# Kernel tuning notes

Measured on AMD Instinct MI355X. Metric: run time of the kernel, lower is better.

The kernel has to match this reference:

```python
import jax, jax.numpy as jnp
import numpy as np
from jax import lax

B, C_IN, C_OUT, K, H, W, NUM = 32, 256, 256, 3, 28, 28, 8


def setup_inputs() -> dict:
    key = jax.random.key(0)
    k1, k2, k3 = jax.random.split(key, 3)
    inputs = jax.random.normal(k1, (B, C_IN, H, W), dtype=jnp.float32)
    inputs_se = jax.random.uniform(k2, (B, NUM), dtype=jnp.float32)
    # weight bank [out*in*k*k, num], init scale sqrt(1/(c*k*k)) as in the module
    scale = np.sqrt(1.0 / (C_IN * K * K)).astype(np.float32)
    weight = jax.random.normal(k3, (C_OUT * C_IN * K * K, NUM), dtype=jnp.float32) * scale
    bias = jnp.zeros((C_OUT,), dtype=jnp.float32)
    return {"inputs": inputs, "inputs_se": inputs_se, "weight": weight, "bias": bias}


def reference(inputs, inputs_se, weight, bias):
    b, c, h, w = inputs.shape
    out_ch = bias.shape[0]
    # per-sample filter generation: [B, num] @ [num, out*in*k*k] -> [B, out, in, k, k]
    wgen = jnp.einsum('bn,on->bo', inputs_se, weight).reshape(b, out_ch, c, K, K)

    def conv_one(x, wk):
        # x: [C,H,W], wk: [O,C,K,K] -> [O,H,W]  (stride 1, padding 1)
        return lax.conv_general_dilated(
            x[None], wk,
            window_strides=(1, 1), padding=[(1, 1), (1, 1)],
            dimension_numbers=('NCHW', 'OIHW', 'NCHW'))[0]

    out = jax.vmap(conv_one)(inputs, wgen)  # [B, O, H, W]
    return out + bias[None, :, None, None]
```

## Files before the change

kernel.cpp:

```cpp
#include <hip/hip_runtime.h>
#include <hip/hip_fp16.h>

#define BB    32
#define CIN   256
#define COUT  256
#define HH    28
#define WW    28
#define NPIX  784
#define HP    30
#define WP    30

#define BM    64
#define BN    128
#define NT    7

#define SLICE_ELEMS 294912
#define WGEN_ELEMS  ((size_t)BB * 2 * SLICE_ELEMS)
#define XPAD_OFF    (WGEN_ELEMS)

#define PREP_GENW  256
#define PREP_GENX  960
#define PREP_GRID  (PREP_GENW + PREP_GENX)

typedef _Float16 f16x8 __attribute__((ext_vector_type(8)));
typedef float    f32x4 __attribute__((ext_vector_type(4)));

static __device__ __forceinline__ ushort f2h_bits(float v) {
    __half h = __float2half(v);
    return *reinterpret_cast<ushort*>(&h);
}

static __device__ __forceinline__ void gll16(const ushort* g, ushort* l) {
    __builtin_amdgcn_global_load_lds(
        (const __attribute__((address_space(1))) unsigned int*)g,
        (__attribute__((address_space(3))) unsigned int*)l, 16, 0, 0);
}

__global__ __launch_bounds__(256) void prep(const float* __restrict__ weight,
                                            const float* __restrict__ se,
                                            const float* __restrict__ x,
                                            ushort* __restrict__ wgen2,
                                            ushort* __restrict__ xpad) {
    __shared__ __align__(16) char smem[29696];
    const int bid = blockIdx.x;
    const int tid = threadIdx.x;

    if (bid < PREP_GENW) {
        const int og  = bid >> 3;
        const int c32 = bid & 7;
        const int ol  = tid >> 5;
        const int cl  = tid & 31;
        const int o   = og * 8 + ol;
        const int c   = c32 * 32 + cl;

        float*  se_sh = (float*)smem;
        ushort* w_lds = (ushort*)(smem + 1024);

        se_sh[tid] = se[tid];

        float4 wr[18];
        const float4* wp = (const float4*)(weight + ((size_t)o * CIN + c) * 72);
#pragma unroll
        for (int i = 0; i < 18; ++i) wr[i] = wp[i];

        const int khw0 = tid >> 5;
        const int q0   = (tid >> 3) & 3;
        const int ol0  = tid & 7;
        const int khw1 = 8;
        const int q1   = (tid >> 3) & 3;
        const int ol1  = tid & 7;
        const int o0   = og * 8 + ol0;
        const int sub0 = (o0 >> 4) & 7, col0 = o0 & 15;
        const int o1   = og * 8 + ol1;
        const int sub1 = (o1 >> 4) & 7, col1 = o1 & 15;
        const int mt0  = o0 >> 7;
        const int dst0 = ((c32 * 9 + khw0) * 512 + sub0 * 64 + q0 * 16 + col0) * 8;
        const int dst1 = ((c32 * 9 + khw1) * 512 + sub1 * 64 + q1 * 16 + col1) * 8;
        const int src0 = (khw0 * 8 + ol0) * 40 + q0 * 8;
        const int src1 = (khw1 * 8 + ol1) * 40 + q1 * 8;

        __syncthreads();

        for (int b = 0; b < BB; ++b) {
            const float s0 = se_sh[b * 8 + 0], s1 = se_sh[b * 8 + 1];
            const float s2 = se_sh[b * 8 + 2], s3 = se_sh[b * 8 + 3];
            const float s4 = se_sh[b * 8 + 4], s5 = se_sh[b * 8 + 5];
            const float s6 = se_sh[b * 8 + 6], s7 = se_sh[b * 8 + 7];
#pragma unroll
            for (int k = 0; k < 9; ++k) {
                const float4 w0 = wr[2 * k + 0];
                const float4 w1 = wr[2 * k + 1];
                const float v = w0.x * s0 + w0.y * s1 + w0.z * s2 + w0.w * s3
                              + w1.x * s4 + w1.y * s5 + w1.z * s6 + w1.w * s7;
                w_lds[(k * 8 + ol) * 40 + cl] = f2h_bits(v);
            }
            __syncthreads();
            ushort* slice_base = wgen2 + (size_t)(b * 2 + mt0) * SLICE_ELEMS;
            *(uint4*)(slice_base + dst0) = *(const uint4*)(w_lds + src0);
            if (tid < 32)
                *(uint4*)(slice_base + dst1) = *(const uint4*)(w_lds + src1);
            __syncthreads();
        }
    } else {
        const int idx = bid - PREP_GENW;
        const int hp  = idx % HP;
        const int b   = idx / HP;
        ushort* row = xpad + ((size_t)b * HP + hp) * WP * CIN;

        if (hp == 0 || hp == HP - 1) {
            uint* r32 = (uint*)row;
            for (int i = tid; i < (WP * CIN) / 2; i += 256) r32[i] = 0u;
            return;
        }
        {
            uint* c0 = (uint*)row;
            uint* c1 = (uint*)(row + (WP - 1) * CIN);
            if (tid < 128)       c0[tid] = 0u;
            else                 c1[tid - 128] = 0u;
        }
        float* lds = (float*)smem;
        const int h = hp - 1;
        const float* xr = x + (size_t)b * CIN * NPIX + h * WW;

        for (int f = tid; f < CIN * WW; f += 256) {
            const int c = f / WW;
            const int w = f % WW;
            lds[c * (WW + 1) + w] = xr[(size_t)c * NPIX + w];
        }
        __syncthreads();
        for (int g2 = tid; g2 < WW * CIN; g2 += 256) {
            const int w = g2 >> 8;
            const int c = g2 & 255;
            row[(w + 1) * CIN + c] = f2h_bits(lds[c * (WW + 1) + w]);
        }
    }
}

#define KOFF(k) (((k) / 3) * 30 + ((k) % 3))

__global__ __launch_bounds__(256, 4) void dconv_mfma(const ushort* __restrict__ wgen2,
                                                     const ushort* __restrict__ xpad,
                                                     const float* __restrict__ bias,
                                                     float* __restrict__ out) {
    const int bid    = blockIdx.x;
    const int g      = bid & 7;
    const int s      = bid >> 3;
    const int t      = s % 14;
    const int nt     = t % 7;
    const int mtl    = t / 7;
    const int slice2 = g + 8 * (s / 14);
    const int b      = slice2 >> 1;
    const int mtH    = slice2 & 1;

    const int tid  = threadIdx.x;
    const int lane = tid & 63;
    const int wave = tid >> 6;
    const int wm   = wave >> 1;
    const int wn   = wave & 1;
    const int col  = lane & 15;
    const int quad = lane >> 4;

    __shared__ ushort Psh[2][7680];

    const int mo   = mtH * 128 + mtl * 64 + wm * 32;
    const int no   = nt * BN + wn * 64;
    const int h_lo = (nt * BN) / WW;

    const f16x8* ag = (const f16x8*)(wgen2 + (size_t)slice2 * SLICE_ELEMS)
                      + (mtl * 4 + wm * 2) * 64 + lane;
    const ushort* xp = xpad + (size_t)b * HP * WP * CIN;

    int p_goff[4], p_loff[4];
    bool p_ok[4];
#pragma unroll
    for (int r = 0; r < 4; ++r) {
        const int j = r * 256 + tid;
        p_ok[r] = (j < 960);
        const int jj  = p_ok[r] ? j : 0;
        const int qc  = jj / 240;
        const int rem = jj % 240;
        const int rr  = rem / 30;
        const int ww  = rem % 30;
        int srow = h_lo + rr;
        if (srow > 29) srow = 29;
        p_goff[r] = (srow * WP + ww) * CIN + qc * 8;
        p_loff[r] = jj * 8;
    }

    int pixbase[4], pst[4];
#pragma unroll
    for (int j = 0; j < 4; ++j) {
        const int p  = no + j * 16 + col;
        pst[j] = p;
        const int pc = p > (NPIX - 1) ? (NPIX - 1) : p;
        pixbase[j] = (pc / WW - h_lo) * 30 + (pc % WW);
    }

    f32x4 acc[2][4];
#pragma unroll
    for (int mi = 0; mi < 2; ++mi)
#pragma unroll
        for (int nj = 0; nj < 4; ++nj)
            acc[mi][nj] = (f32x4){0.f, 0.f, 0.f, 0.f};

#pragma unroll
    for (int r = 0; r < 4; ++r)
        if (p_ok[r]) gll16(xp + p_goff[r], &Psh[0][p_loff[r]]);

    f16x8 afr[3][2];
#pragma unroll
    for (int mi = 0; mi < 2; ++mi) afr[0][mi] = ag[mi * 64];
    {
        const f16x8* a1 = ag + (1 << 9);
#pragma unroll
        for (int mi = 0; mi < 2; ++mi) afr[1][mi] = a1[mi * 64];
    }

    f16x8 bfr[2][4];

    for (int c32 = 0; c32 < 8; ++c32) {
        __syncthreads();

        if (c32 < 7) {
            const int nb = (c32 + 1) & 1;
#pragma unroll
            for (int r = 0; r < 4; ++r)
                if (p_ok[r]) gll16(xp + p_goff[r] + (c32 + 1) * 32,
                                   &Psh[nb][p_loff[r]]);
        }

        const f16x8* Pc = (const f16x8*)Psh[c32 & 1];

#pragma unroll
        for (int j = 0; j < 4; ++j)
            bfr[0][j] = Pc[quad * 240 + pixbase[j] + KOFF(0)];

#pragma unroll
        for (int khw = 0; khw < 9; ++khw) {
            const int st = c32 * 9 + khw;
            int sp = st + 2; if (sp > 71) sp = 71;
            const f16x8* apf = ag + ((size_t)sp << 9);
#pragma unroll
            for (int mi = 0; mi < 2; ++mi)
                afr[(khw + 2) % 3][mi] = apf[mi * 64];
            if (khw < 8) {
#pragma unroll
                for (int j = 0; j < 4; ++j)
                    bfr[(khw + 1) & 1][j] = Pc[quad * 240 + pixbase[j] + KOFF(khw + 1)];
            }
#pragma unroll
            for (int mi = 0; mi < 2; ++mi)
#pragma unroll
                for (int nj = 0; nj < 4; ++nj)
                    acc[mi][nj] = __builtin_amdgcn_mfma_f32_16x16x32_f16(
                        afr[khw % 3][mi], bfr[khw & 1][nj], acc[mi][nj], 0, 0, 0);
        }
    }

    float* ob = out + (size_t)b * COUT * NPIX;
#pragma unroll
    for (int mi = 0; mi < 2; ++mi) {
        const int m = mo + mi * 16 + quad * 4;
        const float4 bv = *(const float4*)(bias + m);
#pragma unroll
        for (int nj = 0; nj < 4; ++nj) {
            const int p = pst[nj];
            if (p < NPIX) {
                ob[(size_t)(m + 0) * NPIX + p] = acc[mi][nj][0] + bv.x;
                ob[(size_t)(m + 1) * NPIX + p] = acc[mi][nj][1] + bv.y;
                ob[(size_t)(m + 2) * NPIX + p] = acc[mi][nj][2] + bv.z;
                ob[(size_t)(m + 3) * NPIX + p] = acc[mi][nj][3] + bv.w;
            }
        }
    }
}

extern "C" void kernel_launch(void* const* d_in, const int* in_sizes, int n_in,
                              void* d_out, int out_size, void* d_ws, size_t ws_size,
                              hipStream_t stream) {
    const float* x      = (const float*)d_in[0];
    const float* se     = (const float*)d_in[1];
    const float* weight = (const float*)d_in[2];
    const float* bias   = (const float*)d_in[3];
    float* out          = (float*)d_out;

    ushort* wgen2 = (ushort*)d_ws;
    ushort* xpad  = (ushort*)d_ws + XPAD_OFF;
    (void)ws_size; (void)in_sizes; (void)n_in; (void)out_size;

    prep<<<dim3(PREP_GRID), dim3(256), 0, stream>>>(weight, se, x, wgen2, xpad);
    dconv_mfma<<<dim3(BB * 4 * NT), dim3(256), 0, stream>>>(wgen2, xpad, bias, out);
}
```

Baseline: 148.5 us.

## Switch conv GEMM to 32x32x16 MFMA with 128x128 block tiles

The conv kernel now uses the 32x32x16 f16 MFMA instead of 16x16x32. The block M tile grows from 64 to 128, which halves the grid, and launch bounds drop to 2 blocks per SM. The weight-generation prep kernel is reworked to write the new fragment layout. It splits batch work across twice as many blocks and double-buffers its LDS staging to drop one barrier per iteration. The aim is more reuse per loaded fragment and denser MFMA issue, at the cost of fewer blocks (448) and lower occupancy.

```diff
diff --git a/kernel.cpp b/kernel.cpp
--- a/kernel.cpp
+++ b/kernel.cpp
@@ -10,7 +10,7 @@
 #define HP    30
 #define WP    30
 
-#define BM    64
+#define BM    128
 #define BN    128
 #define NT    7
 
@@ -18,12 +18,12 @@
 #define WGEN_ELEMS  ((size_t)BB * 2 * SLICE_ELEMS)
 #define XPAD_OFF    (WGEN_ELEMS)
 
-#define PREP_GENW  256
+#define PREP_GENW  512
 #define PREP_GENX  960
 #define PREP_GRID  (PREP_GENW + PREP_GENX)
 
-typedef _Float16 f16x8 __attribute__((ext_vector_type(8)));
-typedef float    f32x4 __attribute__((ext_vector_type(4)));
+typedef _Float16 f16x8  __attribute__((ext_vector_type(8)));
+typedef float    f32x16 __attribute__((ext_vector_type(16)));
 
 static __device__ __forceinline__ ushort f2h_bits(float v) {
     __half h = __float2half(v);
@@ -36,22 +36,26 @@
         (__attribute__((address_space(3))) unsigned int*)l, 16, 0, 0);
 }
 
+#define KOFF(k) (((k) / 3) * 30 + ((k) % 3))
+
 __global__ __launch_bounds__(256) void prep(const float* __restrict__ weight,
                                             const float* __restrict__ se,
                                             const float* __restrict__ x,
-                                            ushort* __restrict__ wgen2,
+                                            ushort* __restrict__ wgen,
                                             ushort* __restrict__ xpad) {
     __shared__ __align__(16) char smem[29696];
     const int bid = blockIdx.x;
     const int tid = threadIdx.x;
 
     if (bid < PREP_GENW) {
-        const int og  = bid >> 3;
+        const int og  = bid >> 4;
+        const int bh  = (bid >> 3) & 1;
         const int c32 = bid & 7;
         const int ol  = tid >> 5;
         const int cl  = tid & 31;
         const int o   = og * 8 + ol;
         const int c   = c32 * 32 + cl;
+        const int mtH = og >> 4;
 
         float*  se_sh = (float*)smem;
         ushort* w_lds = (ushort*)(smem + 1024);
@@ -63,25 +67,28 @@
 #pragma unroll
         for (int i = 0; i < 18; ++i) wr[i] = wp[i];
 
-        const int khw0 = tid >> 5;
-        const int q0   = (tid >> 3) & 3;
-        const int ol0  = tid & 7;
-        const int khw1 = 8;
-        const int q1   = (tid >> 3) & 3;
-        const int ol1  = tid & 7;
-        const int o0   = og * 8 + ol0;
-        const int sub0 = (o0 >> 4) & 7, col0 = o0 & 15;
-        const int o1   = og * 8 + ol1;
-        const int sub1 = (o1 >> 4) & 7, col1 = o1 & 15;
-        const int mt0  = o0 >> 7;
-        const int dst0 = ((c32 * 9 + khw0) * 512 + sub0 * 64 + q0 * 16 + col0) * 8;
-        const int dst1 = ((c32 * 9 + khw1) * 512 + sub1 * 64 + q1 * 16 + col1) * 8;
-        const int src0 = (khw0 * 8 + ol0) * 40 + q0 * 8;
-        const int src1 = (khw1 * 8 + ol1) * 40 + q1 * 8;
+        const int r0    = tid & 31;
+        const int khw0  = tid >> 5;
+        const int ol0   = r0 & 7;
+        const int half0 = (r0 >> 3) & 1;
+        const int s0_   = r0 >> 4;
+        const int sub32 = (og & 15) >> 2;
+        const int lanep = (og & 3) * 8;
+        const int dst0  = ((c32 * 9 + khw0) * 512 + s0_ * 256 + sub32 * 64
+                           + 32 * half0 + lanep + ol0) * 8;
+        const int src0  = (khw0 * 8 + ol0) * 40 + s0_ * 16 + half0 * 8;
+        const int ol1   = tid & 7;
+        const int half1 = (tid >> 3) & 1;
+        const int s1_   = tid >> 4;
+        const int dst1  = ((c32 * 9 + 8) * 512 + s1_ * 256 + sub32 * 64
+                           + 32 * half1 + lanep + ol1) * 8;
+        const int src1  = (8 * 8 + ol1) * 40 + s1_ * 16 + half1 * 8;
 
         __syncthreads();
 
-        for (int b = 0; b < BB; ++b) {
+        for (int bi = 0; bi < 16; ++bi) {
+            const int b   = bh * 16 + bi;
+            const int buf = (bi & 1) * 2880;
             const float s0 = se_sh[b * 8 + 0], s1 = se_sh[b * 8 + 1];
             const float s2 = se_sh[b * 8 + 2], s3 = se_sh[b * 8 + 3];
             const float s4 = se_sh[b * 8 + 4], s5 = se_sh[b * 8 + 5];
@@ -92,14 +99,13 @@
                 const float4 w1 = wr[2 * k + 1];
                 const float v = w0.x * s0 + w0.y * s1 + w0.z * s2 + w0.w * s3
                               + w1.x * s4 + w1.y * s5 + w1.z * s6 + w1.w * s7;
-                w_lds[(k * 8 + ol) * 40 + cl] = f2h_bits(v);
+                w_lds[buf + (k * 8 + ol) * 40 + cl] = f2h_bits(v);
             }
             __syncthreads();
-            ushort* slice_base = wgen2 + (size_t)(b * 2 + mt0) * SLICE_ELEMS;
-            *(uint4*)(slice_base + dst0) = *(const uint4*)(w_lds + src0);
+            ushort* slice_base = wgen + (size_t)(b * 2 + mtH) * SLICE_ELEMS;
+            *(uint4*)(slice_base + dst0) = *(const uint4*)(w_lds + buf + src0);
             if (tid < 32)
-                *(uint4*)(slice_base + dst1) = *(const uint4*)(w_lds + src1);
-            __syncthreads();
+                *(uint4*)(slice_base + dst1) = *(const uint4*)(w_lds + buf + src1);
         }
     } else {
         const int idx = bid - PREP_GENW;
@@ -123,32 +129,28 @@
         const float* xr = x + (size_t)b * CIN * NPIX + h * WW;
 
         for (int f = tid; f < CIN * WW; f += 256) {
-            const int c = f / WW;
-            const int w = f % WW;
-            lds[c * (WW + 1) + w] = xr[(size_t)c * NPIX + w];
+            const int cc = f / WW;
+            const int w  = f % WW;
+            lds[cc * (WW + 1) + w] = xr[(size_t)cc * NPIX + w];
         }
         __syncthreads();
         for (int g2 = tid; g2 < WW * CIN; g2 += 256) {
-            const int w = g2 >> 8;
-            const int c = g2 & 255;
-            row[(w + 1) * CIN + c] = f2h_bits(lds[c * (WW + 1) + w]);
-        }
-    }
-}
-
-#define KOFF(k) (((k) / 3) * 30 + ((k) % 3))
-
-__global__ __launch_bounds__(256, 4) void dconv_mfma(const ushort* __restrict__ wgen2,
+            const int w  = g2 >> 8;
+            const int cc = g2 & 255;
+            row[(w + 1) * CIN + cc] = f2h_bits(lds[cc * (WW + 1) + w]);
+        }
+    }
+}
+
+__global__ __launch_bounds__(256, 2) void dconv_mfma(const ushort* __restrict__ wgen,
                                                      const ushort* __restrict__ xpad,
                                                      const float* __restrict__ bias,
                                                      float* __restrict__ out) {
     const int bid    = blockIdx.x;
     const int g      = bid & 7;
     const int s      = bid >> 3;
-    const int t      = s % 14;
-    const int nt     = t % 7;
-    const int mtl    = t / 7;
-    const int slice2 = g + 8 * (s / 14);
+    const int nt     = s % NT;
+    const int slice2 = g + 8 * (s / NT);
     const int b      = slice2 >> 1;
     const int mtH    = slice2 & 1;
 
@@ -157,17 +159,17 @@
     const int wave = tid >> 6;
     const int wm   = wave >> 1;
     const int wn   = wave & 1;
-    const int col  = lane & 15;
-    const int quad = lane >> 4;
+    const int n5   = lane & 31;
+    const int half = lane >> 5;
 
     __shared__ ushort Psh[2][7680];
 
-    const int mo   = mtH * 128 + mtl * 64 + wm * 32;
+    const int mo   = mtH * 128 + wm * 64;
     const int no   = nt * BN + wn * 64;
     const int h_lo = (nt * BN) / WW;
 
-    const f16x8* ag = (const f16x8*)(wgen2 + (size_t)slice2 * SLICE_ELEMS)
-                      + (mtl * 4 + wm * 2) * 64 + lane;
+    const f16x8* ag = (const f16x8*)(wgen + (size_t)slice2 * SLICE_ELEMS)
+                      + wm * 128 + lane;
     const ushort* xp = xpad + (size_t)b * HP * WP * CIN;
 
     int p_goff[4], p_loff[4];
@@ -187,21 +189,21 @@
         p_loff[r] = jj * 8;
     }
 
-    int pixbase[4], pst[4];
-#pragma unroll
-    for (int j = 0; j < 4; ++j) {
-        const int p  = no + j * 16 + col;
-        pst[j] = p;
+    int pixbase[2], pst[2];
+#pragma unroll
+    for (int nj = 0; nj < 2; ++nj) {
+        const int p  = no + nj * 32 + n5;
+        pst[nj] = p;
         const int pc = p > (NPIX - 1) ? (NPIX - 1) : p;
-        pixbase[j] = (pc / WW - h_lo) * 30 + (pc % WW);
-    }
-
-    f32x4 acc[2][4];
+        pixbase[nj] = (pc / WW - h_lo) * 30 + (pc % WW);
+    }
+
+    f32x16 acc[2][2];
 #pragma unroll
     for (int mi = 0; mi < 2; ++mi)
 #pragma unroll
-        for (int nj = 0; nj < 4; ++nj)
-            acc[mi][nj] = (f32x4){0.f, 0.f, 0.f, 0.f};
+        for (int nj = 0; nj < 2; ++nj)
+            acc[mi][nj] = (f32x16)(0.f);
 
 #pragma unroll
     for (int r = 0; r < 4; ++r)
@@ -209,14 +211,13 @@
 
     f16x8 afr[3][2];
 #pragma unroll
-    for (int mi = 0; mi < 2; ++mi) afr[0][mi] = ag[mi * 64];
-    {
-        const f16x8* a1 = ag + (1 << 9);
-#pragma unroll
-        for (int mi = 0; mi < 2; ++mi) afr[1][mi] = a1[mi * 64];
-    }
-
-    f16x8 bfr[2][4];
+    for (int sl = 0; sl < 2; ++sl) {
+        const f16x8* ap = ag + sl * 256;
+#pragma unroll
+        for (int mi = 0; mi < 2; ++mi) afr[sl][mi] = ap[mi * 64];
+    }
+
+    f16x8 bfr[2][2];
 
     for (int c32 = 0; c32 < 8; ++c32) {
         __syncthreads();
@@ -232,44 +233,49 @@
         const f16x8* Pc = (const f16x8*)Psh[c32 & 1];
 
 #pragma unroll
-        for (int j = 0; j < 4; ++j)
-            bfr[0][j] = Pc[quad * 240 + pixbase[j] + KOFF(0)];
-
-#pragma unroll
-        for (int khw = 0; khw < 9; ++khw) {
-            const int st = c32 * 9 + khw;
-            int sp = st + 2; if (sp > 71) sp = 71;
-            const f16x8* apf = ag + ((size_t)sp << 9);
+        for (int nj = 0; nj < 2; ++nj)
+            bfr[0][nj] = Pc[half * 240 + pixbase[nj]];
+
+#pragma unroll
+        for (int st18 = 0; st18 < 18; ++st18) {
+            const int st = c32 * 18 + st18;
+            int sp = st + 2; if (sp > 143) sp = 143;
+            const f16x8* apf = ag + sp * 256;
 #pragma unroll
             for (int mi = 0; mi < 2; ++mi)
-                afr[(khw + 2) % 3][mi] = apf[mi * 64];
-            if (khw < 8) {
-#pragma unroll
-                for (int j = 0; j < 4; ++j)
-                    bfr[(khw + 1) & 1][j] = Pc[quad * 240 + pixbase[j] + KOFF(khw + 1)];
+                afr[(st18 + 2) % 3][mi] = apf[mi * 64];
+            if (st18 < 17) {
+                const int ns = (st18 + 1) & 1;
+                const int nk = (st18 + 1) >> 1;
+#pragma unroll
+                for (int nj = 0; nj < 2; ++nj)
+                    bfr[ns][nj] = Pc[(ns * 2 + half) * 240 + pixbase[nj] + KOFF(nk)];
             }
 #pragma unroll
             for (int mi = 0; mi < 2; ++mi)
 #pragma unroll
-                for (int nj = 0; nj < 4; ++nj)
-                    acc[mi][nj] = __builtin_amdgcn_mfma_f32_16x16x32_f16(
-                        afr[khw % 3][mi], bfr[khw & 1][nj], acc[mi][nj], 0, 0, 0);
+                for (int nj = 0; nj < 2; ++nj)
+                    acc[mi][nj] = __builtin_amdgcn_mfma_f32_32x32x16_f16(
+                        afr[st18 % 3][mi], bfr[st18 & 1][nj], acc[mi][nj], 0, 0, 0);
         }
     }
 
     float* ob = out + (size_t)b * COUT * NPIX;
 #pragma unroll
     for (int mi = 0; mi < 2; ++mi) {
-        const int m = mo + mi * 16 + quad * 4;
-        const float4 bv = *(const float4*)(bias + m);
-#pragma unroll
-        for (int nj = 0; nj < 4; ++nj) {
-            const int p = pst[nj];
-            if (p < NPIX) {
-                ob[(size_t)(m + 0) * NPIX + p] = acc[mi][nj][0] + bv.x;
-                ob[(size_t)(m + 1) * NPIX + p] = acc[mi][nj][1] + bv.y;
-                ob[(size_t)(m + 2) * NPIX + p] = acc[mi][nj][2] + bv.z;
-                ob[(size_t)(m + 3) * NPIX + p] = acc[mi][nj][3] + bv.w;
+#pragma unroll
+        for (int rg = 0; rg < 4; ++rg) {
+            const int m0 = mo + mi * 32 + 8 * rg + 4 * half;
+            const float4 bv = *(const float4*)(bias + m0);
+#pragma unroll
+            for (int nj = 0; nj < 2; ++nj) {
+                const int p = pst[nj];
+                if (p < NPIX) {
+                    ob[(size_t)(m0 + 0) * NPIX + p] = acc[mi][nj][rg * 4 + 0] + bv.x;
+                    ob[(size_t)(m0 + 1) * NPIX + p] = acc[mi][nj][rg * 4 + 1] + bv.y;
+                    ob[(size_t)(m0 + 2) * NPIX + p] = acc[mi][nj][rg * 4 + 2] + bv.z;
+                    ob[(size_t)(m0 + 3) * NPIX + p] = acc[mi][nj][rg * 4 + 3] + bv.w;
+                }
             }
         }
     }
@@ -284,10 +290,10 @@
     const float* bias   = (const float*)d_in[3];
     float* out          = (float*)d_out;
 
-    ushort* wgen2 = (ushort*)d_ws;
-    ushort* xpad  = (ushort*)d_ws + XPAD_OFF;
+    ushort* wgen = (ushort*)d_ws;
+    ushort* xpad = (ushort*)d_ws + XPAD_OFF;
     (void)ws_size; (void)in_sizes; (void)n_in; (void)out_size;
 
-    prep<<<dim3(PREP_GRID), dim3(256), 0, stream>>>(weight, se, x, wgen2, xpad);
-    dconv_mfma<<<dim3(BB * 4 * NT), dim3(256), 0, stream>>>(wgen2, xpad, bias, out);
-}
+    prep<<<dim3(PREP_GRID), dim3(256), 0, stream>>>(weight, se, x, wgen, xpad);
+    dconv_mfma<<<dim3(BB * 2 * NT), dim3(256), 0, stream>>>(wgen, xpad, bias, out);
+}
```

Result: slower. 177.8 us (+19.7%).
